# Optimization experiments

Measured on AMD Instinct MI355X. Metric: run time of the kernel, lower is better.

Reference implementation:

```python
import jax, jax.numpy as jnp
import numpy as np

LN_EPS = 1e-5

def _layer_norm(x, g, b):
    mu = jnp.mean(x, axis=-1, keepdims=True)
    var = jnp.mean(jnp.square(x - mu), axis=-1, keepdims=True)
    return (x - mu) * jax.lax.rsqrt(var + LN_EPS) * g + b

def _conv(x, src, tgt, N, alphas, ws, W3, W_self, bias, deg_power):
    # alphas, ws: tuples of 3 per-edge [E] arrays (sp, ctx, lat)
    # W3: [3, in, out]; deg_power: [3]
    out = x @ W_self + bias  # self loop + bias, [N, out]
    for c in range(3):
        eff = alphas[c] * ws[c]                                   # [E]
        deg = jnp.ones((N,), x.dtype).at[tgt].add(eff)            # [N]
        dinv = jnp.power(jnp.clip(deg, 1e-6), deg_power[c])       # [N]
        norm = eff * dinv[tgt] * dinv[src]                        # [E]
        h = x @ W3[c]                                             # [N, out] (linear => transform before gather)
        msg = norm[:, None] * h[src]                              # [E, out]
        out = out + jax.ops.segment_sum(msg, tgt, num_segments=N)
    return out

def setup_inputs() -> dict:
    N, E, D, L = 50000, 1000000, 128, 2
    key = jax.random.key(0)
    ks = jax.random.split(key, 16)
    scale = 1.0 / np.sqrt(D)
    inp = {
        "x": jax.random.normal(ks[0], (N, D), jnp.float32),
        "edge_index": jax.random.randint(ks[1], (2, E), 0, N, jnp.int32),
        "alpha_sp": jax.random.uniform(ks[2], (E,), jnp.float32),
        "alpha_ctx": jax.random.uniform(ks[3], (E,), jnp.float32),
        "alpha_lat": jax.random.uniform(ks[4], (E,), jnp.float32),
        "w_sp": jax.random.uniform(ks[5], (E,), jnp.float32),
        "w_ctx": jax.random.uniform(ks[6], (E,), jnp.float32),
        "w_lat": jax.random.uniform(ks[7], (E,), jnp.float32),
        # stacked per-layer params: [L, 3, in, out] for the three channel weights
        "W3": jax.random.normal(ks[8], (L, 3, D, D), jnp.float32) * scale,
        "W_self": jax.random.normal(ks[9], (L, D, D), jnp.float32) * scale,
        "bias": jnp.zeros((L, D), jnp.float32),
        "deg_power": jnp.full((L, 3), -0.5, jnp.float32),
        "ln_g": jnp.ones((D,), jnp.float32),
        "ln_b": jnp.zeros((D,), jnp.float32),
        "num_nodes": N,
    }
    return inp

def reference(x, edge_index, alpha_sp, alpha_ctx, alpha_lat, w_sp, w_ctx, w_lat,
              W3, W_self, bias, deg_power, ln_g, ln_b, num_nodes):
    N = num_nodes
    src, tgt = edge_index[0], edge_index[1]
    alphas = (alpha_sp, alpha_ctx, alpha_lat)
    ws = (w_sp, w_ctx, w_lat)
    L = W3.shape[0]
    h = x
    for i in range(L):
        h = _conv(h, src, tgt, N, alphas, ws, W3[i], W_self[i], bias[i], deg_power[i])
        if i < L - 1:
            h = _layer_norm(h, ln_g, ln_b)
            h = jax.nn.relu(h)
            # dropout: eval mode (identity)
    return h
```

## Files before the change

### kernel.cpp

```cpp
#include <hip/hip_runtime.h>
#include <hip/hip_bf16.h>

typedef short bf16x8 __attribute__((ext_vector_type(8)));
typedef float f32x4 __attribute__((ext_vector_type(4)));

#define BSH 7
#define BK  (1 << BSH)

static inline int cdiv(int a, int b){ return (a + b - 1) / b; }

__device__ __forceinline__ unsigned pack_bf16_hi(float v){
    return ((unsigned)__bfloat16_as_ushort(__float2bfloat16(v))) << 16;
}
__device__ __forceinline__ float bf16hi_to_f32(unsigned bits_hi16){
    return __uint_as_float(bits_hi16);
}

__global__ __launch_bounds__(256) void k_bcnt0(const int* __restrict__ tgt,
                                               int* __restrict__ gcnt, int E, int NB){
    __shared__ int lh[1024];
    int tid = threadIdx.x;
    for (int b = tid; b < 1024; b += 256) lh[b] = 0;
    __syncthreads();
    int c0 = blockIdx.x * 4096;
    #pragma unroll
    for (int u = 0; u < 16; ++u){
        int e = c0 + u * 256 + tid;
        if (e < E) atomicAdd(&lh[tgt[e] >> BSH], 1);
    }
    __syncthreads();
    for (int b = tid; b < NB; b += 256){
        int c = lh[b];
        if (c) atomicAdd(&gcnt[b], c);
    }
}

__global__ __launch_bounds__(256) void k_bscan(const int* __restrict__ gcnt,
                                               int* __restrict__ bbase,
                                               int* __restrict__ gcur,
                                               int* __restrict__ rs,
                                               int N, int E){
    __shared__ int sc[256];
    int tid = threadIdx.x;
    int b0 = tid * 4;
    int v0 = gcnt[b0], v1 = gcnt[b0 + 1], v2 = gcnt[b0 + 2], v3 = gcnt[b0 + 3];
    int t3 = v0 + v1 + v2 + v3;
    sc[tid] = t3;
    __syncthreads();
    for (int off = 1; off < 256; off <<= 1){
        int x = (tid >= off) ? sc[tid - off] : 0;
        __syncthreads();
        sc[tid] += x;
        __syncthreads();
    }
    int ex = sc[tid] - t3;
    bbase[b0]     = ex;
    bbase[b0 + 1] = ex + v0;
    bbase[b0 + 2] = ex + v0 + v1;
    bbase[b0 + 3] = ex + v0 + v1 + v2;
    gcur[b0] = bbase[b0]; gcur[b0 + 1] = bbase[b0 + 1];
    gcur[b0 + 2] = bbase[b0 + 2]; gcur[b0 + 3] = bbase[b0 + 3];
    if (tid == 255) bbase[1024] = sc[255];
    if (tid == 0)   rs[N] = E;
}

__global__ __launch_bounds__(256) void k_bin(
        const int* __restrict__ src, const int* __restrict__ tgt,
        const float* __restrict__ asp, const float* __restrict__ actx,
        const float* __restrict__ alat, const float* __restrict__ wsp,
        const float* __restrict__ wctx, const float* __restrict__ wlat,
        int* __restrict__ gcur, uint4* __restrict__ binned, int E, int NB){
    __shared__ int lh[1024], lc[1024], gb[1024];
    int tid = threadIdx.x;
    int c0 = blockIdx.x * 4096;
    for (int b = tid; b < 1024; b += 256){ lh[b] = 0; lc[b] = 0; }
    __syncthreads();
    #pragma unroll
    for (int u = 0; u < 16; ++u){
        int e = c0 + u * 256 + tid;
        if (e < E) atomicAdd(&lh[tgt[e] >> BSH], 1);
    }
    __syncthreads();
    for (int b = tid; b < NB; b += 256){
        int c = lh[b];
        gb[b] = c ? atomicAdd(&gcur[b], c) : 0;
    }
    __syncthreads();
    #pragma unroll
    for (int u = 0; u < 16; ++u){
        int e = c0 + u * 256 + tid;
        if (e < E){
            int t = tgt[e];
            int b = t >> BSH;
            int p = gb[b] + atomicAdd(&lc[b], 1);
            uint4 o;
            o.x = (unsigned)src[e] | pack_bf16_hi(asp[e] * wsp[e]);
            o.y = (pack_bf16_hi(actx[e] * wctx[e]) >> 16) | pack_bf16_hi(alat[e] * wlat[e]);
            o.z = (unsigned)t;
            o.w = 0u;
            binned[p] = o;
        }
    }
}

__global__ __launch_bounds__(256) void k_bucket(
        const uint4* __restrict__ binned, const int* __restrict__ bbase,
        uint2* __restrict__ effo, int* __restrict__ rs, int N){
    __shared__ int th[128], sc2[128], cur[128];
    int tid = threadIdx.x;
    int b = blockIdx.x;
    int t0 = b << BSH;
    int ebeg = bbase[b], eend = bbase[b + 1];
    if (tid < 128) th[tid] = 0;
    __syncthreads();
    for (int i = ebeg + tid; i < eend; i += 256)
        atomicAdd(&th[(int)binned[i].z - t0], 1);
    __syncthreads();
    int v = (tid < 128) ? th[tid] : 0;
    if (tid < 128) sc2[tid] = v;
    __syncthreads();
    for (int off = 1; off < 128; off <<= 1){
        int x = (tid >= off && tid < 128) ? sc2[tid - off] : 0;
        __syncthreads();
        if (tid < 128) sc2[tid] += x;
        __syncthreads();
    }
    if (tid < 128){
        int exv = sc2[tid] - v;
        cur[tid] = exv;
        int t = t0 + tid;
        if (t < N) rs[t] = ebeg + exv;
    }
    __syncthreads();
    for (int i = ebeg + tid; i < eend; i += 256){
        uint4 r = binned[i];
        int loc = (int)r.z - t0;
        int p = atomicAdd(&cur[loc], 1);
        uint2 o = {r.x, r.y};
        effo[ebeg + p] = o;
    }
}

__global__ __launch_bounds__(256) void k_deg(
        const uint2* __restrict__ effo, const int* __restrict__ rs,
        const float* __restrict__ dp,
        float* __restrict__ dinv_all,
        int N, int L){
    int n = blockIdx.x * 256 + threadIdx.x;
    if (n >= N) return;
    int beg = rs[n], end = rs[n + 1];
    float s0 = 0.f, s1 = 0.f, s2 = 0.f;
    for (int i = beg; i < end; ++i){
        uint2 v = effo[i];
        s0 += bf16hi_to_f32(v.x & 0xFFFF0000u);
        s1 += bf16hi_to_f32(v.y << 16);
        s2 += bf16hi_to_f32(v.y & 0xFFFF0000u);
    }
    float d0 = fmaxf(1.f + s0, 1e-6f);
    float d1 = fmaxf(1.f + s1, 1e-6f);
    float d2 = fmaxf(1.f + s2, 1e-6f);
    for (int l = 0; l < L; ++l){
        size_t base = ((size_t)l * N + n) * 3;
        dinv_all[base + 0] = powf(d0, dp[l * 3 + 0]);
        dinv_all[base + 1] = powf(d1, dp[l * 3 + 1]);
        dinv_all[base + 2] = powf(d2, dp[l * 3 + 2]);
    }
}

__global__ void k_normv(const uint2* __restrict__ effo,
                        const float* __restrict__ dinv_all,
                        uint2* __restrict__ nv, int E, int N, int L){
    int i = blockIdx.x * 256 + threadIdx.x;
    if (i >= L * E) return;
    int l = i / E;
    int e = i - l * E;
    const float* dinv = dinv_all + (size_t)l * N * 3;
    uint2 v = effo[e];
    unsigned s = v.x & 0xFFFFu;
    float e0 = bf16hi_to_f32(v.x & 0xFFFF0000u);
    float e1 = bf16hi_to_f32(v.y << 16);
    float e2 = bf16hi_to_f32(v.y & 0xFFFF0000u);
    float n0 = e0 * dinv[3 * s + 0];
    float n1 = e1 * dinv[3 * s + 1];
    float n2 = e2 * dinv[3 * s + 2];
    uint2 o;
    o.x = s | pack_bf16_hi(n0);
    o.y = (pack_bf16_hi(n1) >> 16) | pack_bf16_hi(n2);
    nv[i] = o;
}

__global__ void k_x2bf(const float* __restrict__ x, __hip_bfloat16* __restrict__ Ap, int n){
    int i = blockIdx.x * 256 + threadIdx.x;
    if (i < n) Ap[(size_t)(i >> 7) * 512 + (i & 127)] = __float2bfloat16(x[i]);
}

__global__ void k_wcat(const float* __restrict__ Wself,
                       const float* __restrict__ W3,
                       __hip_bfloat16* __restrict__ BT,
                       int L){
    int i = blockIdx.x * 256 + threadIdx.x;
    if (i >= L * 65536) return;
    int l = i >> 16, r = i & 65535;
    int j = r >> 9, k = r & 511;
    float v;
    if (k < 128) v = Wself[l * 16384 + k * 128 + j];
    else {
        int c = (k >> 7) - 1, kk = k & 127;
        v = W3[l * 49152 + (c * 128 + kk) * 128 + j];
    }
    BT[i] = __float2bfloat16(v);
}

__global__ __launch_bounds__(256) void k_msg(
        __hip_bfloat16* __restrict__ Ap,
        const uint2* __restrict__ nv,
        const int* __restrict__ rs,
        const float* __restrict__ dinv,
        int N){
    int w = threadIdx.x >> 6, lane = threadIdx.x & 63;
    int t = blockIdx.x * 4 + w;
    if (t >= N) return;
    float ax0 = 0.f, ay0 = 0.f, ax1 = 0.f, ay1 = 0.f, ax2 = 0.f, ay2 = 0.f;
    int beg = rs[t], end = rs[t + 1];
    int i = beg;
    for (; i + 8 <= end; i += 8){
        uint2 m[8];
        #pragma unroll
        for (int u = 0; u < 8; ++u) m[u] = nv[i + u];
        float2 f[8];
        #pragma unroll
        for (int u = 0; u < 8; ++u){
            const __hip_bfloat162* p =
                (const __hip_bfloat162*)(Ap + (size_t)(m[u].x & 0xFFFFu) * 512);
            f[u] = __bfloat1622float2(p[lane]);
        }
        #pragma unroll
        for (int u = 0; u < 8; ++u){
            float n0 = bf16hi_to_f32(m[u].x & 0xFFFF0000u);
            float n1 = bf16hi_to_f32(m[u].y << 16);
            float n2 = bf16hi_to_f32(m[u].y & 0xFFFF0000u);
            ax0 += n0 * f[u].x; ay0 += n0 * f[u].y;
            ax1 += n1 * f[u].x; ay1 += n1 * f[u].y;
            ax2 += n2 * f[u].x; ay2 += n2 * f[u].y;
        }
    }
    for (; i < end; ++i){
        uint2 m = nv[i];
        const __hip_bfloat162* p =
            (const __hip_bfloat162*)(Ap + (size_t)(m.x & 0xFFFFu) * 512);
        float2 fv = __bfloat1622float2(p[lane]);
        float n0 = bf16hi_to_f32(m.x & 0xFFFF0000u);
        float n1 = bf16hi_to_f32(m.y << 16);
        float n2 = bf16hi_to_f32(m.y & 0xFFFF0000u);
        ax0 += n0 * fv.x; ay0 += n0 * fv.y;
        ax1 += n1 * fv.x; ay1 += n1 * fv.y;
        ax2 += n2 * fv.x; ay2 += n2 * fv.y;
    }
    float dt0 = dinv[3 * t], dt1 = dinv[3 * t + 1], dt2 = dinv[3 * t + 2];
    __hip_bfloat162* yo = (__hip_bfloat162*)(Ap + (size_t)t * 512 + 128) + lane;
    float2 r0 = {dt0 * ax0, dt0 * ay0};
    float2 r1 = {dt1 * ax1, dt1 * ay1};
    float2 r2 = {dt2 * ax2, dt2 * ay2};
    yo[0]   = __float22bfloat162_rn(r0);
    yo[64]  = __float22bfloat162_rn(r1);
    yo[128] = __float22bfloat162_rn(r2);
}

__global__ __launch_bounds__(256) void k_gemm(
        const __hip_bfloat16* __restrict__ A,
        const __hip_bfloat16* __restrict__ BT,
        const float* __restrict__ bias,
        float* __restrict__ outbuf,
        int M, int doLN,
        const float* __restrict__ g, const float* __restrict__ b,
        __hip_bfloat16* __restrict__ Ap){
    __shared__ __hip_bfloat16 As[128 * 128];
    __shared__ __hip_bfloat16 Bs[128 * 128];
    const int tid = threadIdx.x;
    const int row0 = blockIdx.x * 128;
    const int w = tid >> 6, lane = tid & 63;
    const int wm = (w & 1) * 64, wn = (w >> 1) * 64;
    const int lm = lane & 15, lq = lane >> 4;

    f32x4 acc[4][4];
    #pragma unroll
    for (int mt = 0; mt < 4; ++mt)
        #pragma unroll
        for (int nt = 0; nt < 4; ++nt)
            acc[mt][nt] = {0.f, 0.f, 0.f, 0.f};

    for (int kt = 0; kt < 4; ++kt){
        #pragma unroll
        for (int it = 0; it < 8; ++it){
            int v = it * 256 + tid;
            int r = v >> 4, c = v & 15;
            int soff = r * 128 + ((c ^ (r & 15)) << 3);
            int4 av = {0, 0, 0, 0};
            if (row0 + r < M)
                av = *(const int4*)(A + (size_t)(row0 + r) * 512 + kt * 128 + (c << 3));
            *(int4*)(&As[soff]) = av;
            int4 bv = *(const int4*)(BT + (size_t)r * 512 + kt * 128 + (c << 3));
            *(int4*)(&Bs[soff]) = bv;
        }
        __syncthreads();

        #pragma unroll
        for (int kk = 0; kk < 4; ++kk){
            int kc = kk * 4 + lq;
            bf16x8 a[4], b2[4];
            #pragma unroll
            for (int mt = 0; mt < 4; ++mt){
                int r = wm + mt * 16 + lm;
                a[mt] = *(const bf16x8*)(&As[r * 128 + ((kc ^ (r & 15)) << 3)]);
            }
            #pragma unroll
            for (int nt = 0; nt < 4; ++nt){
                int r = wn + nt * 16 + lm;
                b2[nt] = *(const bf16x8*)(&Bs[r * 128 + ((kc ^ (r & 15)) << 3)]);
            }
            #pragma unroll
            for (int mt = 0; mt < 4; ++mt)
                #pragma unroll
                for (int nt = 0; nt < 4; ++nt)
                    acc[mt][nt] = __builtin_amdgcn_mfma_f32_16x16x32_bf16(
                        a[mt], b2[nt], acc[mt][nt], 0, 0, 0);
        }
        __syncthreads();
    }

    if (!doLN){
        #pragma unroll
        for (int mt = 0; mt < 4; ++mt){
            #pragma unroll
            for (int nt = 0; nt < 4; ++nt){
                int col = wn + nt * 16 + lm;
                #pragma unroll
                for (int r = 0; r < 4; ++r){
                    int row = row0 + wm + mt * 16 + lq * 4 + r;
                    if (row < M)
                        outbuf[(size_t)row * 128 + col] = acc[mt][nt][r] + bias[col];
                }
            }
        }
    } else {
        float* S1 = (float*)As;
        float* S2 = S1 + 4096;
        float* MS = (float*)Bs;
        const int half = wn >> 6;
        const int slot = half * 16 + lm;
        float bv[4];
        #pragma unroll
        for (int nt = 0; nt < 4; ++nt) bv[nt] = bias[wn + nt * 16 + lm];
        #pragma unroll
        for (int mt = 0; mt < 4; ++mt){
            #pragma unroll
            for (int r = 0; r < 4; ++r){
                int rl = wm + mt * 16 + lq * 4 + r;
                float ps = 0.f, pq = 0.f;
                #pragma unroll
                for (int nt = 0; nt < 4; ++nt){
                    float v = acc[mt][nt][r] + bv[nt];
                    ps += v; pq += v * v;
                }
                S1[rl * 32 + slot] = ps;
                S2[rl * 32 + slot] = pq;
            }
        }
        __syncthreads();
        if (tid < 128){
            float s = 0.f, sq = 0.f;
            #pragma unroll
            for (int j = 0; j < 32; ++j){
                s  += S1[tid * 32 + j];
                sq += S2[tid * 32 + j];
            }
            float mu = s * (1.0f / 128.0f);
            float var = sq * (1.0f / 128.0f) - mu * mu;
            MS[tid] = mu;
            MS[128 + tid] = rsqrtf(var + 1e-5f);
        }
        __syncthreads();
        float gv[4], bbv[4];
        #pragma unroll
        for (int nt = 0; nt < 4; ++nt){
            int col = wn + nt * 16 + lm;
            gv[nt] = g[col]; bbv[nt] = b[col];
        }
        #pragma unroll
        for (int mt = 0; mt < 4; ++mt){
            #pragma unroll
            for (int r = 0; r < 4; ++r){
                int rl = wm + mt * 16 + lq * 4 + r;
                int row = row0 + rl;
                if (row < M){
                    float mu = MS[rl], sc = MS[128 + rl];
                    #pragma unroll
                    for (int nt = 0; nt < 4; ++nt){
                        int col = wn + nt * 16 + lm;
                        float v = acc[mt][nt][r] + bv[nt];
                        float y = fmaxf((v - mu) * sc * gv[nt] + bbv[nt], 0.0f);
                        Ap[(size_t)row * 512 + col] = __float2bfloat16(y);
                    }
                }
            }
        }
    }
}

extern "C" void kernel_launch(void* const* d_in, const int* in_sizes, int n_in,
                              void* d_out, int out_size, void* d_ws, size_t ws_size,
                              hipStream_t stream) {
    const float* x     = (const float*)d_in[0];
    const int*   ei    = (const int*)d_in[1];
    const float* asp   = (const float*)d_in[2];
    const float* actx  = (const float*)d_in[3];
    const float* alat  = (const float*)d_in[4];
    const float* wsp   = (const float*)d_in[5];
    const float* wctx  = (const float*)d_in[6];
    const float* wlat  = (const float*)d_in[7];
    const float* W3    = (const float*)d_in[8];
    const float* Wself = (const float*)d_in[9];
    const float* bias  = (const float*)d_in[10];
    const float* dpow  = (const float*)d_in[11];
    const float* lng   = (const float*)d_in[12];
    const float* lnb   = (const float*)d_in[13];

    const int N = in_sizes[0] / 128;
    const int E = in_sizes[1] / 2;
    const int L = in_sizes[8] / (3 * 128 * 128);
    const int NB = cdiv(N, BK);
    const int* src = ei;
    const int* tgt = ei + E;

    char* p = (char*)d_ws;
    auto alloc = [&](size_t bytes) -> void* {
        void* r = (void*)p;
        p += (bytes + 255) & ~(size_t)255;
        return r;
    };
    int*   rs       = (int*)  alloc((size_t)(N + 1) * 4);
    int*   gcnt     = (int*)  alloc(1024 * 4);
    int*   bbase    = (int*)  alloc(1025 * 4);
    int*   gcur     = (int*)  alloc(1024 * 4);
    uint2* effo     = (uint2*)alloc((size_t)E * 8);
    uint2* nv       = (uint2*)alloc((size_t)L * E * 8);
    float* dinv_all = (float*)alloc((size_t)L * N * 3 * 4);
    __hip_bfloat16* Ap = (__hip_bfloat16*)alloc((size_t)N * 512 * 2);
    __hip_bfloat16* BT = (__hip_bfloat16*)alloc((size_t)L * 128 * 512 * 2);
    uint4* binned = (uint4*)nv;

    hipMemsetAsync(gcnt, 0, 1024 * 4, stream);
    k_bcnt0 <<<cdiv(E, 4096), 256, 0, stream>>>(tgt, gcnt, E, NB);
    k_bscan <<<1, 256, 0, stream>>>(gcnt, bbase, gcur, rs, N, E);
    k_bin   <<<cdiv(E, 4096), 256, 0, stream>>>(src, tgt, asp, actx, alat, wsp, wctx, wlat,
                                                gcur, binned, E, NB);
    k_bucket<<<NB, 256, 0, stream>>>(binned, bbase, effo, rs, N);
    k_deg   <<<cdiv(N, 256), 256, 0, stream>>>(effo, rs, dpow, dinv_all, N, L);
    k_x2bf  <<<cdiv(N * 128, 256), 256, 0, stream>>>(x, Ap, N * 128);
    k_wcat  <<<cdiv(L * 65536, 256), 256, 0, stream>>>(Wself, W3, BT, L);
    k_normv <<<cdiv(L * E, 256), 256, 0, stream>>>(effo, dinv_all, nv, E, N, L);

    for (int l = 0; l < L; ++l){
        int doLN = (l < L - 1) ? 1 : 0;
        const float* dinv_l = dinv_all + (size_t)l * N * 3;
        k_msg <<<cdiv(N, 4), 256, 0, stream>>>(Ap, nv + (size_t)l * E, rs, dinv_l, N);
        k_gemm<<<cdiv(N, 128), 256, 0, stream>>>(Ap, BT + (size_t)l * 65536,
                                                 bias + l * 128, (float*)d_out, N,
                                                 doLN, lng, lnb, Ap);
    }
}
```

Measured before the change: 352.3 us.

## Fuse degree computation into bucketing and apply source norm inside message kernel

Degree sums are accumulated with shared-memory atomics inside k_bucket, which also writes dinv, so the separate k_deg and k_normv kernels and the per-layer normalized edge buffer go away. k_msg now reads raw edge weights and multiplies by a padded float4 dinv of the source on the fly. Each wavefront processes 4 edges at once with 16 lanes loading 8 bf16 each, then reduces across lane groups with shuffles. The binned scratch is aliased onto Ap, which is safe only because k_x2bf runs after k_bucket. The cost is an extra dinv gather per edge in every layer and float atomics in LDS.

```diff
diff --git a/kernel.cpp b/kernel.cpp
--- a/kernel.cpp
+++ b/kernel.cpp
@@ -105,13 +105,18 @@
 
 __global__ __launch_bounds__(256) void k_bucket(
         const uint4* __restrict__ binned, const int* __restrict__ bbase,
-        uint2* __restrict__ effo, int* __restrict__ rs, int N){
+        const float* __restrict__ dp,
+        uint2* __restrict__ effo, int* __restrict__ rs,
+        float* __restrict__ dinv_all,
+        int N, int L){
     __shared__ int th[128], sc2[128], cur[128];
+    __shared__ float sm[384];
     int tid = threadIdx.x;
     int b = blockIdx.x;
     int t0 = b << BSH;
     int ebeg = bbase[b], eend = bbase[b + 1];
     if (tid < 128) th[tid] = 0;
+    for (int j = tid; j < 384; j += 256) sm[j] = 0.f;
     __syncthreads();
     for (int i = ebeg + tid; i < eend; i += 256)
         atomicAdd(&th[(int)binned[i].z - t0], 1);
@@ -138,55 +143,26 @@
         int p = atomicAdd(&cur[loc], 1);
         uint2 o = {r.x, r.y};
         effo[ebeg + p] = o;
-    }
-}
-
-__global__ __launch_bounds__(256) void k_deg(
-        const uint2* __restrict__ effo, const int* __restrict__ rs,
-        const float* __restrict__ dp,
-        float* __restrict__ dinv_all,
-        int N, int L){
-    int n = blockIdx.x * 256 + threadIdx.x;
-    if (n >= N) return;
-    int beg = rs[n], end = rs[n + 1];
-    float s0 = 0.f, s1 = 0.f, s2 = 0.f;
-    for (int i = beg; i < end; ++i){
-        uint2 v = effo[i];
-        s0 += bf16hi_to_f32(v.x & 0xFFFF0000u);
-        s1 += bf16hi_to_f32(v.y << 16);
-        s2 += bf16hi_to_f32(v.y & 0xFFFF0000u);
-    }
-    float d0 = fmaxf(1.f + s0, 1e-6f);
-    float d1 = fmaxf(1.f + s1, 1e-6f);
-    float d2 = fmaxf(1.f + s2, 1e-6f);
-    for (int l = 0; l < L; ++l){
-        size_t base = ((size_t)l * N + n) * 3;
-        dinv_all[base + 0] = powf(d0, dp[l * 3 + 0]);
-        dinv_all[base + 1] = powf(d1, dp[l * 3 + 1]);
-        dinv_all[base + 2] = powf(d2, dp[l * 3 + 2]);
-    }
-}
-
-__global__ void k_normv(const uint2* __restrict__ effo,
-                        const float* __restrict__ dinv_all,
-                        uint2* __restrict__ nv, int E, int N, int L){
-    int i = blockIdx.x * 256 + threadIdx.x;
-    if (i >= L * E) return;
-    int l = i / E;
-    int e = i - l * E;
-    const float* dinv = dinv_all + (size_t)l * N * 3;
-    uint2 v = effo[e];
-    unsigned s = v.x & 0xFFFFu;
-    float e0 = bf16hi_to_f32(v.x & 0xFFFF0000u);
-    float e1 = bf16hi_to_f32(v.y << 16);
-    float e2 = bf16hi_to_f32(v.y & 0xFFFF0000u);
-    float n0 = e0 * dinv[3 * s + 0];
-    float n1 = e1 * dinv[3 * s + 1];
-    float n2 = e2 * dinv[3 * s + 2];
-    uint2 o;
-    o.x = s | pack_bf16_hi(n0);
-    o.y = (pack_bf16_hi(n1) >> 16) | pack_bf16_hi(n2);
-    nv[i] = o;
+        atomicAdd(&sm[loc * 3 + 0], bf16hi_to_f32(r.x & 0xFFFF0000u));
+        atomicAdd(&sm[loc * 3 + 1], bf16hi_to_f32(r.y << 16));
+        atomicAdd(&sm[loc * 3 + 2], bf16hi_to_f32(r.y & 0xFFFF0000u));
+    }
+    __syncthreads();
+    if (tid < 128){
+        int t = t0 + tid;
+        if (t < N){
+            float d0 = fmaxf(1.f + sm[tid * 3 + 0], 1e-6f);
+            float d1 = fmaxf(1.f + sm[tid * 3 + 1], 1e-6f);
+            float d2 = fmaxf(1.f + sm[tid * 3 + 2], 1e-6f);
+            for (int l = 0; l < L; ++l){
+                size_t base = ((size_t)l * N + t) * 4;
+                dinv_all[base + 0] = powf(d0, dp[l * 3 + 0]);
+                dinv_all[base + 1] = powf(d1, dp[l * 3 + 1]);
+                dinv_all[base + 2] = powf(d2, dp[l * 3 + 2]);
+                dinv_all[base + 3] = 0.f;
+            }
+        }
+    }
 }
 
 __global__ void k_x2bf(const float* __restrict__ x, __hip_bfloat16* __restrict__ Ap, int n){
@@ -213,57 +189,91 @@
 
 __global__ __launch_bounds__(256) void k_msg(
         __hip_bfloat16* __restrict__ Ap,
-        const uint2* __restrict__ nv,
+        const uint2* __restrict__ effo,
         const int* __restrict__ rs,
-        const float* __restrict__ dinv,
+        const float4* __restrict__ dinv4,
         int N){
     int w = threadIdx.x >> 6, lane = threadIdx.x & 63;
+    int g = lane >> 4, c = lane & 15;
     int t = blockIdx.x * 4 + w;
     if (t >= N) return;
-    float ax0 = 0.f, ay0 = 0.f, ax1 = 0.f, ay1 = 0.f, ax2 = 0.f, ay2 = 0.f;
     int beg = rs[t], end = rs[t + 1];
-    int i = beg;
-    for (; i + 8 <= end; i += 8){
-        uint2 m[8];
-        #pragma unroll
-        for (int u = 0; u < 8; ++u) m[u] = nv[i + u];
-        float2 f[8];
-        #pragma unroll
-        for (int u = 0; u < 8; ++u){
-            const __hip_bfloat162* p =
-                (const __hip_bfloat162*)(Ap + (size_t)(m[u].x & 0xFFFFu) * 512);
-            f[u] = __bfloat1622float2(p[lane]);
-        }
-        #pragma unroll
-        for (int u = 0; u < 8; ++u){
-            float n0 = bf16hi_to_f32(m[u].x & 0xFFFF0000u);
-            float n1 = bf16hi_to_f32(m[u].y << 16);
-            float n2 = bf16hi_to_f32(m[u].y & 0xFFFF0000u);
-            ax0 += n0 * f[u].x; ay0 += n0 * f[u].y;
-            ax1 += n1 * f[u].x; ay1 += n1 * f[u].y;
-            ax2 += n2 * f[u].x; ay2 += n2 * f[u].y;
-        }
-    }
-    for (; i < end; ++i){
-        uint2 m = nv[i];
-        const __hip_bfloat162* p =
-            (const __hip_bfloat162*)(Ap + (size_t)(m.x & 0xFFFFu) * 512);
-        float2 fv = __bfloat1622float2(p[lane]);
-        float n0 = bf16hi_to_f32(m.x & 0xFFFF0000u);
-        float n1 = bf16hi_to_f32(m.y << 16);
-        float n2 = bf16hi_to_f32(m.y & 0xFFFF0000u);
-        ax0 += n0 * fv.x; ay0 += n0 * fv.y;
-        ax1 += n1 * fv.x; ay1 += n1 * fv.y;
-        ax2 += n2 * fv.x; ay2 += n2 * fv.y;
-    }
-    float dt0 = dinv[3 * t], dt1 = dinv[3 * t + 1], dt2 = dinv[3 * t + 2];
-    __hip_bfloat162* yo = (__hip_bfloat162*)(Ap + (size_t)t * 512 + 128) + lane;
-    float2 r0 = {dt0 * ax0, dt0 * ay0};
-    float2 r1 = {dt1 * ax1, dt1 * ay1};
-    float2 r2 = {dt2 * ax2, dt2 * ay2};
-    yo[0]   = __float22bfloat162_rn(r0);
-    yo[64]  = __float22bfloat162_rn(r1);
-    yo[128] = __float22bfloat162_rn(r2);
+    if (beg == end){
+        if (g < 3){
+            bf16x8 z = {0, 0, 0, 0, 0, 0, 0, 0};
+            *(bf16x8*)(Ap + (size_t)t * 512 + 128 + g * 128 + c * 8) = z;
+        }
+        return;
+    }
+    float a0[8], a1[8], a2[8];
+    #pragma unroll
+    for (int j = 0; j < 8; ++j){ a0[j] = 0.f; a1[j] = 0.f; a2[j] = 0.f; }
+
+    for (int i = beg; i < end; i += 8){
+        int e0 = i + g, e1 = i + 4 + g;
+        bool p0 = e0 < end, p1 = e1 < end;
+        uint2 m0 = effo[p0 ? e0 : beg];
+        uint2 m1 = effo[p1 ? e1 : beg];
+        int s0 = (int)(m0.x & 0xFFFFu);
+        int s1 = (int)(m1.x & 0xFFFFu);
+        float4 d0 = dinv4[s0];
+        float4 d1 = dinv4[s1];
+        bf16x8 x0 = *(const bf16x8*)(Ap + (size_t)s0 * 512 + c * 8);
+        bf16x8 x1 = *(const bf16x8*)(Ap + (size_t)s1 * 512 + c * 8);
+        float n00 = 0.f, n01 = 0.f, n02 = 0.f, n10 = 0.f, n11 = 0.f, n12 = 0.f;
+        if (p0){
+            n00 = bf16hi_to_f32(m0.x & 0xFFFF0000u) * d0.x;
+            n01 = bf16hi_to_f32(m0.y << 16)         * d0.y;
+            n02 = bf16hi_to_f32(m0.y & 0xFFFF0000u) * d0.z;
+        }
+        if (p1){
+            n10 = bf16hi_to_f32(m1.x & 0xFFFF0000u) * d1.x;
+            n11 = bf16hi_to_f32(m1.y << 16)         * d1.y;
+            n12 = bf16hi_to_f32(m1.y & 0xFFFF0000u) * d1.z;
+        }
+        const unsigned* u0 = (const unsigned*)&x0;
+        const unsigned* u1 = (const unsigned*)&x1;
+        #pragma unroll
+        for (int k2 = 0; k2 < 4; ++k2){
+            float f0a = __uint_as_float(u0[k2] << 16);
+            float f0b = __uint_as_float(u0[k2] & 0xFFFF0000u);
+            a0[2*k2]   += n00 * f0a; a0[2*k2+1] += n00 * f0b;
+            a1[2*k2]   += n01 * f0a; a1[2*k2+1] += n01 * f0b;
+            a2[2*k2]   += n02 * f0a; a2[2*k2+1] += n02 * f0b;
+            float f1a = __uint_as_float(u1[k2] << 16);
+            float f1b = __uint_as_float(u1[k2] & 0xFFFF0000u);
+            a0[2*k2]   += n10 * f1a; a0[2*k2+1] += n10 * f1b;
+            a1[2*k2]   += n11 * f1a; a1[2*k2+1] += n11 * f1b;
+            a2[2*k2]   += n12 * f1a; a2[2*k2+1] += n12 * f1b;
+        }
+    }
+
+    #pragma unroll
+    for (int j = 0; j < 8; ++j){
+        a0[j] += __shfl_xor(a0[j], 16); a0[j] += __shfl_xor(a0[j], 32);
+        a1[j] += __shfl_xor(a1[j], 16); a1[j] += __shfl_xor(a1[j], 32);
+        a2[j] += __shfl_xor(a2[j], 16); a2[j] += __shfl_xor(a2[j], 32);
+    }
+
+    float4 dt = dinv4[t];
+    float r[8];
+    if (g == 0){
+        #pragma unroll
+        for (int j = 0; j < 8; ++j) r[j] = dt.x * a0[j];
+    } else if (g == 1){
+        #pragma unroll
+        for (int j = 0; j < 8; ++j) r[j] = dt.y * a1[j];
+    } else if (g == 2){
+        #pragma unroll
+        for (int j = 0; j < 8; ++j) r[j] = dt.z * a2[j];
+    }
+    if (g < 3){
+        bf16x8 o;
+        #pragma unroll
+        for (int j = 0; j < 8; ++j)
+            o[j] = (short)__bfloat16_as_ushort(__float2bfloat16(r[j]));
+        *(bf16x8*)(Ap + (size_t)t * 512 + 128 + g * 128 + c * 8) = o;
+    }
 }
 
 __global__ __launch_bounds__(256) void k_gemm(
@@ -443,27 +453,24 @@
     int*   bbase    = (int*)  alloc(1025 * 4);
     int*   gcur     = (int*)  alloc(1024 * 4);
     uint2* effo     = (uint2*)alloc((size_t)E * 8);
-    uint2* nv       = (uint2*)alloc((size_t)L * E * 8);
-    float* dinv_all = (float*)alloc((size_t)L * N * 3 * 4);
+    float* dinv_all = (float*)alloc((size_t)L * N * 4 * 4);
     __hip_bfloat16* Ap = (__hip_bfloat16*)alloc((size_t)N * 512 * 2);
     __hip_bfloat16* BT = (__hip_bfloat16*)alloc((size_t)L * 128 * 512 * 2);
-    uint4* binned = (uint4*)nv;
+    uint4* binned = (uint4*)Ap;
 
     hipMemsetAsync(gcnt, 0, 1024 * 4, stream);
     k_bcnt0 <<<cdiv(E, 4096), 256, 0, stream>>>(tgt, gcnt, E, NB);
     k_bscan <<<1, 256, 0, stream>>>(gcnt, bbase, gcur, rs, N, E);
     k_bin   <<<cdiv(E, 4096), 256, 0, stream>>>(src, tgt, asp, actx, alat, wsp, wctx, wlat,
                                                 gcur, binned, E, NB);
-    k_bucket<<<NB, 256, 0, stream>>>(binned, bbase, effo, rs, N);
-    k_deg   <<<cdiv(N, 256), 256, 0, stream>>>(effo, rs, dpow, dinv_all, N, L);
+    k_bucket<<<NB, 256, 0, stream>>>(binned, bbase, dpow, effo, rs, dinv_all, N, L);
     k_x2bf  <<<cdiv(N * 128, 256), 256, 0, stream>>>(x, Ap, N * 128);
     k_wcat  <<<cdiv(L * 65536, 256), 256, 0, stream>>>(Wself, W3, BT, L);
-    k_normv <<<cdiv(L * E, 256), 256, 0, stream>>>(effo, dinv_all, nv, E, N, L);
 
     for (int l = 0; l < L; ++l){
         int doLN = (l < L - 1) ? 1 : 0;
-        const float* dinv_l = dinv_all + (size_t)l * N * 3;
-        k_msg <<<cdiv(N, 4), 256, 0, stream>>>(Ap, nv + (size_t)l * E, rs, dinv_l, N);
+        const float4* dinv_l = (const float4*)dinv_all + (size_t)l * N;
+        k_msg <<<cdiv(N, 4), 256, 0, stream>>>(Ap, effo, rs, dinv_l, N);
         k_gemm<<<cdiv(N, 128), 256, 0, stream>>>(Ap, BT + (size_t)l * 65536,
                                                  bias + l * 128, (float*)d_out, N,
                                                  doLN, lng, lnb, Ap);
```

New measurement: 347.5 us. About the same (-1.3%).

## Fuse degree computation into bucketing and apply source dinv inside message kernel

Applied to the files above, without the earlier changes.

Degree sums are now accumulated with shared-memory atomics inside k_bucket, and dinv is written there in a padded float4 layout, so the separate k_deg pass is gone. The per-layer precomputed normalized edge array (k_normv) is removed; k_msg instead gathers the source node's dinv as a float4 and multiplies it on the fly. The x and weight conversion kernels are merged into one launch, and the binned scratch buffer now aliases Ap. The trade is fewer launches and no 2·E·8-byte normalized-edge write, paid for by an extra random float4 gather per edge inside the hot message kernel.

```diff
diff --git a/kernel.cpp b/kernel.cpp
--- a/kernel.cpp
+++ b/kernel.cpp
@@ -105,13 +105,18 @@
 
 __global__ __launch_bounds__(256) void k_bucket(
         const uint4* __restrict__ binned, const int* __restrict__ bbase,
-        uint2* __restrict__ effo, int* __restrict__ rs, int N){
+        const float* __restrict__ dp,
+        uint2* __restrict__ effo, int* __restrict__ rs,
+        float* __restrict__ dinv_all,
+        int N, int L){
     __shared__ int th[128], sc2[128], cur[128];
+    __shared__ float sm[384];
     int tid = threadIdx.x;
     int b = blockIdx.x;
     int t0 = b << BSH;
     int ebeg = bbase[b], eend = bbase[b + 1];
     if (tid < 128) th[tid] = 0;
+    for (int j = tid; j < 384; j += 256) sm[j] = 0.f;
     __syncthreads();
     for (int i = ebeg + tid; i < eend; i += 256)
         atomicAdd(&th[(int)binned[i].z - t0], 1);
@@ -138,84 +143,55 @@
         int p = atomicAdd(&cur[loc], 1);
         uint2 o = {r.x, r.y};
         effo[ebeg + p] = o;
-    }
-}
-
-__global__ __launch_bounds__(256) void k_deg(
-        const uint2* __restrict__ effo, const int* __restrict__ rs,
-        const float* __restrict__ dp,
-        float* __restrict__ dinv_all,
-        int N, int L){
-    int n = blockIdx.x * 256 + threadIdx.x;
-    if (n >= N) return;
-    int beg = rs[n], end = rs[n + 1];
-    float s0 = 0.f, s1 = 0.f, s2 = 0.f;
-    for (int i = beg; i < end; ++i){
-        uint2 v = effo[i];
-        s0 += bf16hi_to_f32(v.x & 0xFFFF0000u);
-        s1 += bf16hi_to_f32(v.y << 16);
-        s2 += bf16hi_to_f32(v.y & 0xFFFF0000u);
-    }
-    float d0 = fmaxf(1.f + s0, 1e-6f);
-    float d1 = fmaxf(1.f + s1, 1e-6f);
-    float d2 = fmaxf(1.f + s2, 1e-6f);
-    for (int l = 0; l < L; ++l){
-        size_t base = ((size_t)l * N + n) * 3;
-        dinv_all[base + 0] = powf(d0, dp[l * 3 + 0]);
-        dinv_all[base + 1] = powf(d1, dp[l * 3 + 1]);
-        dinv_all[base + 2] = powf(d2, dp[l * 3 + 2]);
-    }
-}
-
-__global__ void k_normv(const uint2* __restrict__ effo,
-                        const float* __restrict__ dinv_all,
-                        uint2* __restrict__ nv, int E, int N, int L){
+        atomicAdd(&sm[loc * 3 + 0], bf16hi_to_f32(r.x & 0xFFFF0000u));
+        atomicAdd(&sm[loc * 3 + 1], bf16hi_to_f32(r.y << 16));
+        atomicAdd(&sm[loc * 3 + 2], bf16hi_to_f32(r.y & 0xFFFF0000u));
+    }
+    __syncthreads();
+    if (tid < 128){
+        int t = t0 + tid;
+        if (t < N){
+            float d0 = fmaxf(1.f + sm[tid * 3 + 0], 1e-6f);
+            float d1 = fmaxf(1.f + sm[tid * 3 + 1], 1e-6f);
+            float d2 = fmaxf(1.f + sm[tid * 3 + 2], 1e-6f);
+            for (int l = 0; l < L; ++l){
+                size_t base = ((size_t)l * N + t) * 4;
+                dinv_all[base + 0] = powf(d0, dp[l * 3 + 0]);
+                dinv_all[base + 1] = powf(d1, dp[l * 3 + 1]);
+                dinv_all[base + 2] = powf(d2, dp[l * 3 + 2]);
+                dinv_all[base + 3] = 0.f;
+            }
+        }
+    }
+}
+
+__global__ void k_prep(const float* __restrict__ x, __hip_bfloat16* __restrict__ Ap,
+                       const float* __restrict__ Wself, const float* __restrict__ W3,
+                       __hip_bfloat16* __restrict__ BT, int nx, int nw){
     int i = blockIdx.x * 256 + threadIdx.x;
-    if (i >= L * E) return;
-    int l = i / E;
-    int e = i - l * E;
-    const float* dinv = dinv_all + (size_t)l * N * 3;
-    uint2 v = effo[e];
-    unsigned s = v.x & 0xFFFFu;
-    float e0 = bf16hi_to_f32(v.x & 0xFFFF0000u);
-    float e1 = bf16hi_to_f32(v.y << 16);
-    float e2 = bf16hi_to_f32(v.y & 0xFFFF0000u);
-    float n0 = e0 * dinv[3 * s + 0];
-    float n1 = e1 * dinv[3 * s + 1];
-    float n2 = e2 * dinv[3 * s + 2];
-    uint2 o;
-    o.x = s | pack_bf16_hi(n0);
-    o.y = (pack_bf16_hi(n1) >> 16) | pack_bf16_hi(n2);
-    nv[i] = o;
-}
-
-__global__ void k_x2bf(const float* __restrict__ x, __hip_bfloat16* __restrict__ Ap, int n){
-    int i = blockIdx.x * 256 + threadIdx.x;
-    if (i < n) Ap[(size_t)(i >> 7) * 512 + (i & 127)] = __float2bfloat16(x[i]);
-}
-
-__global__ void k_wcat(const float* __restrict__ Wself,
-                       const float* __restrict__ W3,
-                       __hip_bfloat16* __restrict__ BT,
-                       int L){
-    int i = blockIdx.x * 256 + threadIdx.x;
-    if (i >= L * 65536) return;
-    int l = i >> 16, r = i & 65535;
-    int j = r >> 9, k = r & 511;
-    float v;
-    if (k < 128) v = Wself[l * 16384 + k * 128 + j];
-    else {
-        int c = (k >> 7) - 1, kk = k & 127;
-        v = W3[l * 49152 + (c * 128 + kk) * 128 + j];
-    }
-    BT[i] = __float2bfloat16(v);
+    if (i < nx){
+        Ap[(size_t)(i >> 7) * 512 + (i & 127)] = __float2bfloat16(x[i]);
+    } else {
+        int q = i - nx;
+        if (q < nw){
+            int l = q >> 16, r = q & 65535;
+            int j = r >> 9, k = r & 511;
+            float v;
+            if (k < 128) v = Wself[l * 16384 + k * 128 + j];
+            else {
+                int c = (k >> 7) - 1, kk = k & 127;
+                v = W3[l * 49152 + (c * 128 + kk) * 128 + j];
+            }
+            BT[q] = __float2bfloat16(v);
+        }
+    }
 }
 
 __global__ __launch_bounds__(256) void k_msg(
         __hip_bfloat16* __restrict__ Ap,
-        const uint2* __restrict__ nv,
+        const uint2* __restrict__ effo,
         const int* __restrict__ rs,
-        const float* __restrict__ dinv,
+        const float4* __restrict__ dinv4,
         int N){
     int w = threadIdx.x >> 6, lane = threadIdx.x & 63;
     int t = blockIdx.x * 4 + w;
@@ -226,7 +202,7 @@
     for (; i + 8 <= end; i += 8){
         uint2 m[8];
         #pragma unroll
-        for (int u = 0; u < 8; ++u) m[u] = nv[i + u];
+        for (int u = 0; u < 8; ++u) m[u] = effo[i + u];
         float2 f[8];
         #pragma unroll
         for (int u = 0; u < 8; ++u){
@@ -236,31 +212,33 @@
         }
         #pragma unroll
         for (int u = 0; u < 8; ++u){
-            float n0 = bf16hi_to_f32(m[u].x & 0xFFFF0000u);
-            float n1 = bf16hi_to_f32(m[u].y << 16);
-            float n2 = bf16hi_to_f32(m[u].y & 0xFFFF0000u);
+            float4 d = dinv4[m[u].x & 0xFFFFu];
+            float n0 = bf16hi_to_f32(m[u].x & 0xFFFF0000u) * d.x;
+            float n1 = bf16hi_to_f32(m[u].y << 16)         * d.y;
+            float n2 = bf16hi_to_f32(m[u].y & 0xFFFF0000u) * d.z;
             ax0 += n0 * f[u].x; ay0 += n0 * f[u].y;
             ax1 += n1 * f[u].x; ay1 += n1 * f[u].y;
             ax2 += n2 * f[u].x; ay2 += n2 * f[u].y;
         }
     }
     for (; i < end; ++i){
-        uint2 m = nv[i];
+        uint2 m = effo[i];
         const __hip_bfloat162* p =
             (const __hip_bfloat162*)(Ap + (size_t)(m.x & 0xFFFFu) * 512);
         float2 fv = __bfloat1622float2(p[lane]);
-        float n0 = bf16hi_to_f32(m.x & 0xFFFF0000u);
-        float n1 = bf16hi_to_f32(m.y << 16);
-        float n2 = bf16hi_to_f32(m.y & 0xFFFF0000u);
+        float4 d = dinv4[m.x & 0xFFFFu];
+        float n0 = bf16hi_to_f32(m.x & 0xFFFF0000u) * d.x;
+        float n1 = bf16hi_to_f32(m.y << 16)         * d.y;
+        float n2 = bf16hi_to_f32(m.y & 0xFFFF0000u) * d.z;
         ax0 += n0 * fv.x; ay0 += n0 * fv.y;
         ax1 += n1 * fv.x; ay1 += n1 * fv.y;
         ax2 += n2 * fv.x; ay2 += n2 * fv.y;
     }
-    float dt0 = dinv[3 * t], dt1 = dinv[3 * t + 1], dt2 = dinv[3 * t + 2];
+    float4 dt = dinv4[t];
     __hip_bfloat162* yo = (__hip_bfloat162*)(Ap + (size_t)t * 512 + 128) + lane;
-    float2 r0 = {dt0 * ax0, dt0 * ay0};
-    float2 r1 = {dt1 * ax1, dt1 * ay1};
-    float2 r2 = {dt2 * ax2, dt2 * ay2};
+    float2 r0 = {dt.x * ax0, dt.x * ay0};
+    float2 r1 = {dt.y * ax1, dt.y * ay1};
+    float2 r2 = {dt.z * ax2, dt.z * ay2};
     yo[0]   = __float22bfloat162_rn(r0);
     yo[64]  = __float22bfloat162_rn(r1);
     yo[128] = __float22bfloat162_rn(r2);
@@ -443,27 +421,26 @@
     int*   bbase    = (int*)  alloc(1025 * 4);
     int*   gcur     = (int*)  alloc(1024 * 4);
     uint2* effo     = (uint2*)alloc((size_t)E * 8);
-    uint2* nv       = (uint2*)alloc((size_t)L * E * 8);
-    float* dinv_all = (float*)alloc((size_t)L * N * 3 * 4);
+    float* dinv_all = (float*)alloc((size_t)L * N * 4 * 4);
     __hip_bfloat16* Ap = (__hip_bfloat16*)alloc((size_t)N * 512 * 2);
     __hip_bfloat16* BT = (__hip_bfloat16*)alloc((size_t)L * 128 * 512 * 2);
-    uint4* binned = (uint4*)nv;
+    uint4* binned = (uint4*)Ap;
 
     hipMemsetAsync(gcnt, 0, 1024 * 4, stream);
     k_bcnt0 <<<cdiv(E, 4096), 256, 0, stream>>>(tgt, gcnt, E, NB);
     k_bscan <<<1, 256, 0, stream>>>(gcnt, bbase, gcur, rs, N, E);
     k_bin   <<<cdiv(E, 4096), 256, 0, stream>>>(src, tgt, asp, actx, alat, wsp, wctx, wlat,
                                                 gcur, binned, E, NB);
-    k_bucket<<<NB, 256, 0, stream>>>(binned, bbase, effo, rs, N);
-    k_deg   <<<cdiv(N, 256), 256, 0, stream>>>(effo, rs, dpow, dinv_all, N, L);
-    k_x2bf  <<<cdiv(N * 128, 256), 256, 0, stream>>>(x, Ap, N * 128);
-    k_wcat  <<<cdiv(L * 65536, 256), 256, 0, stream>>>(Wself, W3, BT, L);
-    k_normv <<<cdiv(L * E, 256), 256, 0, stream>>>(effo, dinv_all, nv, E, N, L);
+    k_bucket<<<NB, 256, 0, stream>>>(binned, bbase, dpow, effo, rs, dinv_all, N, L);
+    {
+        int nx = N * 128, nw = L * 65536;
+        k_prep<<<cdiv(nx + nw, 256), 256, 0, stream>>>(x, Ap, Wself, W3, BT, nx, nw);
+    }
 
     for (int l = 0; l < L; ++l){
         int doLN = (l < L - 1) ? 1 : 0;
-        const float* dinv_l = dinv_all + (size_t)l * N * 3;
-        k_msg <<<cdiv(N, 4), 256, 0, stream>>>(Ap, nv + (size_t)l * E, rs, dinv_l, N);
+        const float4* dinv_l = (const float4*)dinv_all + (size_t)l * N;
+        k_msg <<<cdiv(N, 4), 256, 0, stream>>>(Ap, effo, rs, dinv_l, N);
         k_gemm<<<cdiv(N, 128), 256, 0, stream>>>(Ap, BT + (size_t)l * 65536,
                                                  bias + l * 128, (float*)d_out, N,
                                                  doLN, lng, lnb, Ap);
```

After: 381.3 us. 1.08x slower.

## Fuse degree computation into bucket sort, split activation buffers, merge prep kernels

Applied to the files above, without the earlier changes.

Degree sums are now accumulated with shared-memory atomics inside the bucket kernel, which removes the separate k_deg pass over the edge list. The x-to-bf16 and weight-transpose kernels are merged into a single launch. The combined 512-wide activation buffer is split into a compact 128-wide x buffer and a 384-wide message buffer, so the gather in k_msg reads densely packed 256-byte rows. This improves cache locality for the random gathers, at the cost of a branching A-load in the GEMM and float shared atomics whose summation order is nondeterministic.

```diff
diff --git a/kernel.cpp b/kernel.cpp
--- a/kernel.cpp
+++ b/kernel.cpp
@@ -105,13 +105,18 @@
 
 __global__ __launch_bounds__(256) void k_bucket(
         const uint4* __restrict__ binned, const int* __restrict__ bbase,
-        uint2* __restrict__ effo, int* __restrict__ rs, int N){
+        const float* __restrict__ dp,
+        uint2* __restrict__ effo, int* __restrict__ rs,
+        float* __restrict__ dinv_all,
+        int N, int L){
     __shared__ int th[128], sc2[128], cur[128];
+    __shared__ float sm[384];
     int tid = threadIdx.x;
     int b = blockIdx.x;
     int t0 = b << BSH;
     int ebeg = bbase[b], eend = bbase[b + 1];
     if (tid < 128) th[tid] = 0;
+    for (int j = tid; j < 384; j += 256) sm[j] = 0.f;
     __syncthreads();
     for (int i = ebeg + tid; i < eend; i += 256)
         atomicAdd(&th[(int)binned[i].z - t0], 1);
@@ -138,32 +143,24 @@
         int p = atomicAdd(&cur[loc], 1);
         uint2 o = {r.x, r.y};
         effo[ebeg + p] = o;
-    }
-}
-
-__global__ __launch_bounds__(256) void k_deg(
-        const uint2* __restrict__ effo, const int* __restrict__ rs,
-        const float* __restrict__ dp,
-        float* __restrict__ dinv_all,
-        int N, int L){
-    int n = blockIdx.x * 256 + threadIdx.x;
-    if (n >= N) return;
-    int beg = rs[n], end = rs[n + 1];
-    float s0 = 0.f, s1 = 0.f, s2 = 0.f;
-    for (int i = beg; i < end; ++i){
-        uint2 v = effo[i];
-        s0 += bf16hi_to_f32(v.x & 0xFFFF0000u);
-        s1 += bf16hi_to_f32(v.y << 16);
-        s2 += bf16hi_to_f32(v.y & 0xFFFF0000u);
-    }
-    float d0 = fmaxf(1.f + s0, 1e-6f);
-    float d1 = fmaxf(1.f + s1, 1e-6f);
-    float d2 = fmaxf(1.f + s2, 1e-6f);
-    for (int l = 0; l < L; ++l){
-        size_t base = ((size_t)l * N + n) * 3;
-        dinv_all[base + 0] = powf(d0, dp[l * 3 + 0]);
-        dinv_all[base + 1] = powf(d1, dp[l * 3 + 1]);
-        dinv_all[base + 2] = powf(d2, dp[l * 3 + 2]);
+        atomicAdd(&sm[loc * 3 + 0], bf16hi_to_f32(r.x & 0xFFFF0000u));
+        atomicAdd(&sm[loc * 3 + 1], bf16hi_to_f32(r.y << 16));
+        atomicAdd(&sm[loc * 3 + 2], bf16hi_to_f32(r.y & 0xFFFF0000u));
+    }
+    __syncthreads();
+    if (tid < 128){
+        int t = t0 + tid;
+        if (t < N){
+            float d0 = fmaxf(1.f + sm[tid * 3 + 0], 1e-6f);
+            float d1 = fmaxf(1.f + sm[tid * 3 + 1], 1e-6f);
+            float d2 = fmaxf(1.f + sm[tid * 3 + 2], 1e-6f);
+            for (int l = 0; l < L; ++l){
+                size_t base = ((size_t)l * N + t) * 3;
+                dinv_all[base + 0] = powf(d0, dp[l * 3 + 0]);
+                dinv_all[base + 1] = powf(d1, dp[l * 3 + 1]);
+                dinv_all[base + 2] = powf(d2, dp[l * 3 + 2]);
+            }
+        }
     }
 }
 
@@ -189,30 +186,31 @@
     nv[i] = o;
 }
 
-__global__ void k_x2bf(const float* __restrict__ x, __hip_bfloat16* __restrict__ Ap, int n){
+__global__ void k_prep(const float* __restrict__ x, __hip_bfloat16* __restrict__ xg,
+                       const float* __restrict__ Wself, const float* __restrict__ W3,
+                       __hip_bfloat16* __restrict__ BT, int nx, int nw){
     int i = blockIdx.x * 256 + threadIdx.x;
-    if (i < n) Ap[(size_t)(i >> 7) * 512 + (i & 127)] = __float2bfloat16(x[i]);
-}
-
-__global__ void k_wcat(const float* __restrict__ Wself,
-                       const float* __restrict__ W3,
-                       __hip_bfloat16* __restrict__ BT,
-                       int L){
-    int i = blockIdx.x * 256 + threadIdx.x;
-    if (i >= L * 65536) return;
-    int l = i >> 16, r = i & 65535;
-    int j = r >> 9, k = r & 511;
-    float v;
-    if (k < 128) v = Wself[l * 16384 + k * 128 + j];
-    else {
-        int c = (k >> 7) - 1, kk = k & 127;
-        v = W3[l * 49152 + (c * 128 + kk) * 128 + j];
-    }
-    BT[i] = __float2bfloat16(v);
+    if (i < nx){
+        xg[i] = __float2bfloat16(x[i]);
+    } else {
+        int q = i - nx;
+        if (q < nw){
+            int l = q >> 16, r = q & 65535;
+            int j = r >> 9, k = r & 511;
+            float v;
+            if (k < 128) v = Wself[l * 16384 + k * 128 + j];
+            else {
+                int c = (k >> 7) - 1, kk = k & 127;
+                v = W3[l * 49152 + (c * 128 + kk) * 128 + j];
+            }
+            BT[q] = __float2bfloat16(v);
+        }
+    }
 }
 
 __global__ __launch_bounds__(256) void k_msg(
-        __hip_bfloat16* __restrict__ Ap,
+        const __hip_bfloat16* __restrict__ xg,
+        __hip_bfloat16* __restrict__ Yg,
         const uint2* __restrict__ nv,
         const int* __restrict__ rs,
         const float* __restrict__ dinv,
@@ -231,7 +229,7 @@
         #pragma unroll
         for (int u = 0; u < 8; ++u){
             const __hip_bfloat162* p =
-                (const __hip_bfloat162*)(Ap + (size_t)(m[u].x & 0xFFFFu) * 512);
+                (const __hip_bfloat162*)(xg + (size_t)(m[u].x & 0xFFFFu) * 128);
             f[u] = __bfloat1622float2(p[lane]);
         }
         #pragma unroll
@@ -247,7 +245,7 @@
     for (; i < end; ++i){
         uint2 m = nv[i];
         const __hip_bfloat162* p =
-            (const __hip_bfloat162*)(Ap + (size_t)(m.x & 0xFFFFu) * 512);
+            (const __hip_bfloat162*)(xg + (size_t)(m.x & 0xFFFFu) * 128);
         float2 fv = __bfloat1622float2(p[lane]);
         float n0 = bf16hi_to_f32(m.x & 0xFFFF0000u);
         float n1 = bf16hi_to_f32(m.y << 16);
@@ -257,7 +255,7 @@
         ax2 += n2 * fv.x; ay2 += n2 * fv.y;
     }
     float dt0 = dinv[3 * t], dt1 = dinv[3 * t + 1], dt2 = dinv[3 * t + 2];
-    __hip_bfloat162* yo = (__hip_bfloat162*)(Ap + (size_t)t * 512 + 128) + lane;
+    __hip_bfloat162* yo = (__hip_bfloat162*)(Yg + (size_t)t * 384) + lane;
     float2 r0 = {dt0 * ax0, dt0 * ay0};
     float2 r1 = {dt1 * ax1, dt1 * ay1};
     float2 r2 = {dt2 * ax2, dt2 * ay2};
@@ -267,13 +265,13 @@
 }
 
 __global__ __launch_bounds__(256) void k_gemm(
-        const __hip_bfloat16* __restrict__ A,
+        const __hip_bfloat16* __restrict__ Yg,
         const __hip_bfloat16* __restrict__ BT,
         const float* __restrict__ bias,
         float* __restrict__ outbuf,
         int M, int doLN,
         const float* __restrict__ g, const float* __restrict__ b,
-        __hip_bfloat16* __restrict__ Ap){
+        __hip_bfloat16* __restrict__ xg){
     __shared__ __hip_bfloat16 As[128 * 128];
     __shared__ __hip_bfloat16 Bs[128 * 128];
     const int tid = threadIdx.x;
@@ -296,8 +294,13 @@
             int r = v >> 4, c = v & 15;
             int soff = r * 128 + ((c ^ (r & 15)) << 3);
             int4 av = {0, 0, 0, 0};
-            if (row0 + r < M)
-                av = *(const int4*)(A + (size_t)(row0 + r) * 512 + kt * 128 + (c << 3));
+            if (row0 + r < M){
+                if (kt == 0)
+                    av = *(const int4*)(xg + (size_t)(row0 + r) * 128 + (c << 3));
+                else
+                    av = *(const int4*)(Yg + (size_t)(row0 + r) * 384
+                                        + (kt - 1) * 128 + (c << 3));
+            }
             *(int4*)(&As[soff]) = av;
             int4 bv = *(const int4*)(BT + (size_t)r * 512 + kt * 128 + (c << 3));
             *(int4*)(&Bs[soff]) = bv;
@@ -399,7 +402,7 @@
                         int col = wn + nt * 16 + lm;
                         float v = acc[mt][nt][r] + bv[nt];
                         float y = fmaxf((v - mu) * sc * gv[nt] + bbv[nt], 0.0f);
-                        Ap[(size_t)row * 512 + col] = __float2bfloat16(y);
+                        xg[(size_t)row * 128 + col] = __float2bfloat16(y);
                     }
                 }
             }
@@ -443,9 +446,11 @@
     int*   bbase    = (int*)  alloc(1025 * 4);
     int*   gcur     = (int*)  alloc(1024 * 4);
     uint2* effo     = (uint2*)alloc((size_t)E * 8);
-    uint2* nv       = (uint2*)alloc((size_t)L * E * 8);
+    size_t nv_bytes = (size_t)L * E * 8, bn_bytes = (size_t)E * 16;
+    uint2* nv       = (uint2*)alloc(nv_bytes > bn_bytes ? nv_bytes : bn_bytes);
     float* dinv_all = (float*)alloc((size_t)L * N * 3 * 4);
-    __hip_bfloat16* Ap = (__hip_bfloat16*)alloc((size_t)N * 512 * 2);
+    __hip_bfloat16* xg = (__hip_bfloat16*)alloc((size_t)N * 128 * 2);
+    __hip_bfloat16* Yg = (__hip_bfloat16*)alloc((size_t)N * 384 * 2);
     __hip_bfloat16* BT = (__hip_bfloat16*)alloc((size_t)L * 128 * 512 * 2);
     uint4* binned = (uint4*)nv;
 
@@ -454,18 +459,19 @@
     k_bscan <<<1, 256, 0, stream>>>(gcnt, bbase, gcur, rs, N, E);
     k_bin   <<<cdiv(E, 4096), 256, 0, stream>>>(src, tgt, asp, actx, alat, wsp, wctx, wlat,
                                                 gcur, binned, E, NB);
-    k_bucket<<<NB, 256, 0, stream>>>(binned, bbase, effo, rs, N);
-    k_deg   <<<cdiv(N, 256), 256, 0, stream>>>(effo, rs, dpow, dinv_all, N, L);
-    k_x2bf  <<<cdiv(N * 128, 256), 256, 0, stream>>>(x, Ap, N * 128);
-    k_wcat  <<<cdiv(L * 65536, 256), 256, 0, stream>>>(Wself, W3, BT, L);
+    k_bucket<<<NB, 256, 0, stream>>>(binned, bbase, dpow, effo, rs, dinv_all, N, L);
     k_normv <<<cdiv(L * E, 256), 256, 0, stream>>>(effo, dinv_all, nv, E, N, L);
+    {
+        int nx = N * 128, nw = L * 65536;
+        k_prep<<<cdiv(nx + nw, 256), 256, 0, stream>>>(x, xg, Wself, W3, BT, nx, nw);
+    }
 
     for (int l = 0; l < L; ++l){
         int doLN = (l < L - 1) ? 1 : 0;
         const float* dinv_l = dinv_all + (size_t)l * N * 3;
-        k_msg <<<cdiv(N, 4), 256, 0, stream>>>(Ap, nv + (size_t)l * E, rs, dinv_l, N);
-        k_gemm<<<cdiv(N, 128), 256, 0, stream>>>(Ap, BT + (size_t)l * 65536,
+        k_msg <<<cdiv(N, 4), 256, 0, stream>>>(xg, Yg, nv + (size_t)l * E, rs, dinv_l, N);
+        k_gemm<<<cdiv(N, 128), 256, 0, stream>>>(Yg, BT + (size_t)l * 65536,
                                                  bias + l * 128, (float*)d_out, N,
-                                                 doLN, lng, lnb, Ap);
-    }
-}
+                                                 doLN, lng, lnb, xg);
+    }
+}
```

After: 351.7 us. No clear change (-0.2%).
